# Kernel tuning notes

Hardware: AMD Instinct MI355X
Metric: run time of the kernel (lower is better)

## Reference

```python
import jax, jax.numpy as jnp
import numpy as np

P, B, N, M, D_LAT = 4, 32, 2048, 512, 128
BETA = 1e-3
BIG = 1e9  # sentinel for masked-out pairwise distances


def quat_to_rotmat(q):
    # q: (..., 4) quaternion (w, x, y, z), normalized then converted
    q = q / jnp.linalg.norm(q, axis=-1, keepdims=True)
    w, x, y, z = q[..., 0], q[..., 1], q[..., 2], q[..., 3]
    R = jnp.stack([
        1 - 2 * (y * y + z * z), 2 * (x * y - w * z), 2 * (x * z + w * y),
        2 * (x * y + w * z), 1 - 2 * (x * x + z * z), 2 * (y * z - w * x),
        2 * (x * z - w * y), 2 * (y * z + w * x), 1 - 2 * (x * x + y * y),
    ], axis=-1)
    return R.reshape(q.shape[:-1] + (3, 3))


def setup_inputs() -> dict:
    key = jax.random.key(0)
    ks = jax.random.split(key, 8)
    return {
        'ipt': jax.random.normal(ks[0], (B, N, 3), jnp.float32),
        'opt': jax.random.normal(ks[1], (P, B, M, 3), jnp.float32),
        'trans': jax.random.normal(ks[2], (P, B, 3), jnp.float32),
        'rots': jax.random.normal(ks[3], (P, B, 4), jnp.float32),
        'probs': jax.random.uniform(ks[4], (P, B, 1), jnp.float32),
        'idx': jax.random.randint(ks[5], (B, N), 0, P),
        'mu': jax.random.normal(ks[6], (B, D_LAT), jnp.float32),
        'logvar': jax.random.normal(ks[7], (B, D_LAT), jnp.float32),
    }


def _parts_distance(ipt, opt, trans, rots, probs, idx):
    # Masked, fully-batched equivalent of the original python double loop:
    # index_select by (idx==i) + _remove_zero_rows are expressed as boolean
    # masks; empty part/sample combinations are excluded via `valid`.
    chamfer_d = 0.0
    coverage = 0.0
    quality = 0.0
    num = 0.0
    nonzero_x = jnp.any(ipt != 0, axis=-1)  # (B, N)
    for i in range(P):  # fixed small part count, structurally distinct slices
        y = opt[i]                                   # (B, M, 3)
        mask_y = jnp.any(y != 0, axis=-1)            # (B, M) _remove_zero_rows
        mx = (idx == i) & nonzero_x                  # (B, N) part selection
        # transform_to_primitives_centric_system: x_local = R (x - t)
        R = quat_to_rotmat(rots[i])                  # (B, 3, 3)
        x = jnp.einsum('bij,bnj->bni', R, ipt - trans[i][:, None, :])
        # pairwise squared distances, (B, N, M)
        D = jnp.sum((x[:, :, None, :] - y[:, None, :, :]) ** 2, axis=-1)
        nx = jnp.sum(mx, axis=-1)                    # (B,)
        ny = jnp.sum(mask_y, axis=-1)                # (B,)
        # quality: mean over valid x of min distance to valid y
        qual = jnp.sum(jnp.where(mx, jnp.min(jnp.where(mask_y[:, None, :], D, BIG), axis=-1), 0.0), axis=-1) / jnp.maximum(nx, 1)
        # coverage: mean over valid y of min distance to valid x
        cov = jnp.sum(jnp.where(mask_y, jnp.min(jnp.where(mx[:, :, None], D, BIG), axis=-2), 0.0), axis=-1) / jnp.maximum(ny, 1)
        cd = qual + cov                              # symmetric chamfer
        valid = (nx > 0) & (ny > 0)                  # x.size(0)!=0 and y.size(0)!=0
        w = jnp.where(valid, probs[i][:, 0], 0.0)    # prob-weighted sum over batch
        n = jnp.sum(valid).astype(jnp.float32)
        has = (n > 0).astype(jnp.float32)
        inv_n = has / jnp.maximum(n, 1.0)
        chamfer_d = chamfer_d + jnp.sum(w * cd) * inv_n
        coverage = coverage + jnp.sum(w * cov) * inv_n
        quality = quality + jnp.sum(w * qual) * inv_n
        num = num + has
    inv_num = 1.0 / jnp.maximum(num, 1.0)
    return chamfer_d * inv_num, coverage * inv_num, quality * inv_num


def KL(mu, logvar):
    # standard VAE KL: sum over latent, mean over batch
    return -0.5 * jnp.sum(1.0 + logvar - mu ** 2 - jnp.exp(logvar)) / mu.shape[0]


def reference(ipt, opt, trans, rots, probs, idx, mu, logvar):
    cds, covs, quals = _parts_distance(ipt, opt, trans, rots, probs, idx)
    kld = KL(mu, logvar)
    return (cds + BETA * kld, cds, covs, quals, kld)
```

## Files before the change

### kernel.cpp

```cpp
#include <hip/hip_runtime.h>
#include <math.h>

#define PP 4
#define BB 32
#define NN 2048
#define MM 512
#define DLAT 128
#define BETA_C 1e-3f
#define BIGV 1e9f
#define SENT 1e8f
#define THREADS 256

__device__ float g_ws[4 * PP * BB];

template<int SLOTS>
__device__ __forceinline__ float quality_pass(
    const float* __restrict__ syx, const float* __restrict__ syy, const float* __restrict__ syz,
    const float* __restrict__ sxx, const float* __restrict__ sxy, const float* __restrict__ sxz,
    int nx, int base, int tid)
{
    float px[SLOTS], py[SLOTS], pz[SLOTS], mna[SLOTS], mnb[SLOTS];
    bool act[SLOTS];
#pragma unroll
    for (int s = 0; s < SLOTS; ++s) {
        int k = base + s * THREADS + tid;
        act[s] = (k < nx);
        px[s] = act[s] ? sxx[k] : SENT;
        py[s] = act[s] ? sxy[k] : SENT;
        pz[s] = act[s] ? sxz[k] : SENT;
        mna[s] = BIGV; mnb[s] = BIGV;
    }
    for (int m = 0; m < MM; m += 4) {
        float4 yx = *reinterpret_cast<const float4*>(syx + m);
        float4 yy = *reinterpret_cast<const float4*>(syy + m);
        float4 yz = *reinterpret_cast<const float4*>(syz + m);
#pragma unroll
        for (int s = 0; s < SLOTS; ++s) {
            float dx0 = px[s] - yx.x, dy0 = py[s] - yy.x, dz0 = pz[s] - yz.x;
            float dx1 = px[s] - yx.y, dy1 = py[s] - yy.y, dz1 = pz[s] - yz.y;
            float dx2 = px[s] - yx.z, dy2 = py[s] - yy.z, dz2 = pz[s] - yz.z;
            float dx3 = px[s] - yx.w, dy3 = py[s] - yy.w, dz3 = pz[s] - yz.w;
            float d0 = dx0 * dx0 + dy0 * dy0 + dz0 * dz0;
            float d1 = dx1 * dx1 + dy1 * dy1 + dz1 * dz1;
            float d2 = dx2 * dx2 + dy2 * dy2 + dz2 * dz2;
            float d3 = dx3 * dx3 + dy3 * dy3 + dz3 * dz3;
            mna[s] = fminf(mna[s], fminf(d0, d1));
            mnb[s] = fminf(mnb[s], fminf(d2, d3));
        }
    }
    float sum = 0.0f;
#pragma unroll
    for (int s = 0; s < SLOTS; ++s)
        if (act[s]) sum += fminf(mna[s], mnb[s]);
    return sum;
}

__device__ __forceinline__ float coverage_pass(
    const float* __restrict__ syx, const float* __restrict__ syy, const float* __restrict__ syz,
    const float* __restrict__ sxx, const float* __restrict__ sxy, const float* __restrict__ sxz,
    int nx4, int tid)
{
    float qx[2], qy[2], qz[2], mna[2], mnb[2];
#pragma unroll
    for (int s = 0; s < 2; ++s) {
        int m = s * THREADS + tid;
        qx[s] = syx[m]; qy[s] = syy[m]; qz[s] = syz[m];
        mna[s] = BIGV; mnb[s] = BIGV;
    }
    for (int k = 0; k < nx4; k += 4) {
        float4 xx = *reinterpret_cast<const float4*>(sxx + k);
        float4 xy = *reinterpret_cast<const float4*>(sxy + k);
        float4 xz = *reinterpret_cast<const float4*>(sxz + k);
#pragma unroll
        for (int s = 0; s < 2; ++s) {
            float dx0 = qx[s] - xx.x, dy0 = qy[s] - xy.x, dz0 = qz[s] - xz.x;
            float dx1 = qx[s] - xx.y, dy1 = qy[s] - xy.y, dz1 = qz[s] - xz.y;
            float dx2 = qx[s] - xx.z, dy2 = qy[s] - xy.z, dz2 = qz[s] - xz.z;
            float dx3 = qx[s] - xx.w, dy3 = qy[s] - xy.w, dz3 = qz[s] - xz.w;
            float d0 = dx0 * dx0 + dy0 * dy0 + dz0 * dz0;
            float d1 = dx1 * dx1 + dy1 * dy1 + dz1 * dz1;
            float d2 = dx2 * dx2 + dy2 * dy2 + dz2 * dz2;
            float d3 = dx3 * dx3 + dy3 * dy3 + dz3 * dz3;
            mna[s] = fminf(mna[s], fminf(d0, d1));
            mnb[s] = fminf(mnb[s], fminf(d2, d3));
        }
    }
    float sum = 0.0f;
#pragma unroll
    for (int s = 0; s < 2; ++s)
        if (qx[s] != SENT)
            sum += fminf(mna[s], mnb[s]);
    return sum;
}

__global__ __launch_bounds__(THREADS) void parts_kernel(
    const float* __restrict__ ipt,
    const float* __restrict__ opt,
    const float* __restrict__ trans,
    const float* __restrict__ rots,
    const int*   __restrict__ idx)
{
    const int b = blockIdx.x;
    const int i = blockIdx.y;
    const int phase = blockIdx.z;
    const int tid = threadIdx.x;

    __shared__ float Rm[12];
    __shared__ int s_nx, s_ny;
    __shared__ __align__(16) float syx[MM], syy[MM], syz[MM];
    __shared__ __align__(16) float sxx[NN], sxy[NN], sxz[NN];
    __shared__ float red[THREADS / 64];

    if (tid == 0) {
        s_nx = 0;
        s_ny = 0;
        const float* q = rots + (i * BB + b) * 4;
        float qw = q[0], qx = q[1], qy = q[2], qz = q[3];
        float inv = 1.0f / sqrtf(qw * qw + qx * qx + qy * qy + qz * qz);
        qw *= inv; qx *= inv; qy *= inv; qz *= inv;
        Rm[0] = 1.0f - 2.0f * (qy * qy + qz * qz);
        Rm[1] = 2.0f * (qx * qy - qw * qz);
        Rm[2] = 2.0f * (qx * qz + qw * qy);
        Rm[3] = 2.0f * (qx * qy + qw * qz);
        Rm[4] = 1.0f - 2.0f * (qx * qx + qz * qz);
        Rm[5] = 2.0f * (qy * qz - qw * qx);
        Rm[6] = 2.0f * (qx * qz - qw * qy);
        Rm[7] = 2.0f * (qy * qz + qw * qx);
        Rm[8] = 1.0f - 2.0f * (qx * qx + qy * qy);
        const float* t = trans + (i * BB + b) * 3;
        Rm[9] = t[0]; Rm[10] = t[1]; Rm[11] = t[2];
    }
    __syncthreads();

    int cnt = 0;
    for (int m = tid; m < MM; m += THREADS) {
        const float* y = opt + (((size_t)i * BB + b) * MM + m) * 3;
        float yx = y[0], yy = y[1], yz = y[2];
        bool v = (yx != 0.0f) | (yy != 0.0f) | (yz != 0.0f);
        if (v) cnt++;
        else { yx = SENT; yy = SENT; yz = SENT; }
        syx[m] = yx; syy[m] = yy; syz[m] = yz;
    }
    if (cnt) atomicAdd(&s_ny, cnt);

    const float R0 = Rm[0], R1 = Rm[1], R2 = Rm[2];
    const float R3 = Rm[3], R4 = Rm[4], R5 = Rm[5];
    const float R6 = Rm[6], R7 = Rm[7], R8 = Rm[8];
    const float t0 = Rm[9], t1 = Rm[10], t2 = Rm[11];
    for (int n = tid; n < NN; n += THREADS) {
        const float* p = ipt + ((size_t)b * NN + n) * 3;
        float px = p[0], py = p[1], pz = p[2];
        bool nz = (px != 0.0f) | (py != 0.0f) | (pz != 0.0f);
        if (nz && idx[b * NN + n] == i) {
            px -= t0; py -= t1; pz -= t2;
            int pos = atomicAdd(&s_nx, 1);
            sxx[pos] = R0 * px + R1 * py + R2 * pz;
            sxy[pos] = R3 * px + R4 * py + R5 * pz;
            sxz[pos] = R6 * px + R7 * py + R8 * pz;
        }
    }
    __syncthreads();
    const int nx = s_nx;
    const int ny = s_ny;
    const int nx4 = (nx + 3) & ~3;
    if (tid < nx4 - nx) {
        sxx[nx + tid] = SENT; sxy[nx + tid] = SENT; sxz[nx + tid] = SENT;
    }
    __syncthreads();

    float sum;
    if (phase == 0) {
        if (nx <= 2 * THREADS) {
            sum = quality_pass<2>(syx, syy, syz, sxx, sxy, sxz, nx, 0, tid);
        } else {
            sum = quality_pass<3>(syx, syy, syz, sxx, sxy, sxz, nx, 0, tid);
            for (int k0 = 3 * THREADS; k0 < nx; k0 += THREADS)
                sum += quality_pass<1>(syx, syy, syz, sxx, sxy, sxz, nx, k0, tid);
        }
    } else {
        sum = coverage_pass(syx, syy, syz, sxx, sxy, sxz, nx4, tid);
    }

    for (int off = 32; off > 0; off >>= 1) sum += __shfl_down(sum, off);
    if ((tid & 63) == 0) red[tid >> 6] = sum;
    __syncthreads();
    if (tid == 0) {
        float tot = 0.0f;
        for (int w = 0; w < THREADS / 64; ++w) tot += red[w];
        int pb = i * BB + b;
        if (phase == 0) {
            g_ws[pb] = tot;
            g_ws[2 * PP * BB + pb] = (float)nx;
        } else {
            g_ws[PP * BB + pb] = tot;
            g_ws[3 * PP * BB + pb] = (float)ny;
        }
    }
}

__global__ __launch_bounds__(256) void finalize_kernel(
    const float* __restrict__ probs,
    const float* __restrict__ mu,
    const float* __restrict__ logvar,
    float* __restrict__ out)
{
    const int tid = threadIdx.x;
    __shared__ float red[4];
    __shared__ float s_wq[PP * BB], s_wc[PP * BB], s_val[PP * BB];

    float kls = 0.0f;
    for (int t = tid; t < BB * DLAT; t += 256) {
        float m_ = mu[t], lv = logvar[t];
        kls += 1.0f + lv - m_ * m_ - expf(lv);
    }
    for (int off = 32; off > 0; off >>= 1) kls += __shfl_down(kls, off);
    if ((tid & 63) == 0) red[tid >> 6] = kls;

    if (tid < PP * BB) {
        float qs = g_ws[tid];
        float cs = g_ws[PP * BB + tid];
        float nxf = g_ws[2 * PP * BB + tid];
        float nyf = g_ws[3 * PP * BB + tid];
        bool valid = (nxf > 0.0f) && (nyf > 0.0f);
        float w = valid ? probs[tid] : 0.0f;
        s_wq[tid] = w * (qs / fmaxf(nxf, 1.0f));
        s_wc[tid] = w * (cs / fmaxf(nyf, 1.0f));
        s_val[tid] = valid ? 1.0f : 0.0f;
    }
    __syncthreads();

    if (tid == 0) {
        float kld = -0.5f * (red[0] + red[1] + red[2] + red[3]) / (float)BB;
        float ch = 0.0f, cov = 0.0f, qu = 0.0f, num = 0.0f;
        for (int i = 0; i < PP; ++i) {
            float sq = 0.0f, sc = 0.0f, n = 0.0f;
            for (int bb = 0; bb < BB; ++bb) {
                sq += s_wq[i * BB + bb];
                sc += s_wc[i * BB + bb];
                n += s_val[i * BB + bb];
            }
            float has = (n > 0.0f) ? 1.0f : 0.0f;
            float invn = has / fmaxf(n, 1.0f);
            qu += sq * invn;
            cov += sc * invn;
            ch += (sq + sc) * invn;
            num += has;
        }
        float invnum = 1.0f / fmaxf(num, 1.0f);
        float cds = ch * invnum;
        out[0] = cds + BETA_C * kld;
        out[1] = cds;
        out[2] = cov * invnum;
        out[3] = qu * invnum;
        out[4] = kld;
    }
}

extern "C" void kernel_launch(void* const* d_in, const int* in_sizes, int n_in,
                              void* d_out, int out_size, void* d_ws, size_t ws_size,
                              hipStream_t stream) {
    const float* ipt    = (const float*)d_in[0];
    const float* opt    = (const float*)d_in[1];
    const float* trans  = (const float*)d_in[2];
    const float* rots   = (const float*)d_in[3];
    const float* probs  = (const float*)d_in[4];
    const int*   idx    = (const int*)d_in[5];
    const float* mu     = (const float*)d_in[6];
    const float* logvar = (const float*)d_in[7];
    float* out = (float*)d_out;
    (void)d_ws; (void)ws_size; (void)in_sizes; (void)n_in; (void)out_size;

    dim3 grid(BB, PP, 2);
    parts_kernel<<<grid, THREADS, 0, stream>>>(ipt, opt, trans, rots, idx);
    finalize_kernel<<<1, 256, 0, stream>>>(probs, mu, logvar, out);
}
```

Before: 110.2 us.

## Split quality and coverage passes into chunks for more blocks

Each (part, batch) pair's quality pass now covers half of the input points and each coverage pass covers half of the output points. This doubles the grid to 512 blocks to fill more compute units, and the partial sums and counts are combined in the finalize kernel. In exchange every block redundantly reloads and filters the inputs, and coverage blocks still scan all gathered points.

```diff
diff --git a/kernel.cpp b/kernel.cpp
--- a/kernel.cpp
+++ b/kernel.cpp
@@ -3,6 +3,7 @@
 
 #define PP 4
 #define BB 32
+#define PB (PP * BB)
 #define NN 2048
 #define MM 512
 #define DLAT 128
@@ -10,8 +11,11 @@
 #define BIGV 1e9f
 #define SENT 1e8f
 #define THREADS 256
-
-__device__ float g_ws[4 * PP * BB];
+#define NCHUNK 2
+#define QCH (NN / NCHUNK)
+#define CCH (MM / NCHUNK)
+
+__device__ float g_ws[8 * PB];
 
 template<int SLOTS>
 __device__ __forceinline__ float quality_pass(
@@ -55,44 +59,6 @@
     return sum;
 }
 
-__device__ __forceinline__ float coverage_pass(
-    const float* __restrict__ syx, const float* __restrict__ syy, const float* __restrict__ syz,
-    const float* __restrict__ sxx, const float* __restrict__ sxy, const float* __restrict__ sxz,
-    int nx4, int tid)
-{
-    float qx[2], qy[2], qz[2], mna[2], mnb[2];
-#pragma unroll
-    for (int s = 0; s < 2; ++s) {
-        int m = s * THREADS + tid;
-        qx[s] = syx[m]; qy[s] = syy[m]; qz[s] = syz[m];
-        mna[s] = BIGV; mnb[s] = BIGV;
-    }
-    for (int k = 0; k < nx4; k += 4) {
-        float4 xx = *reinterpret_cast<const float4*>(sxx + k);
-        float4 xy = *reinterpret_cast<const float4*>(sxy + k);
-        float4 xz = *reinterpret_cast<const float4*>(sxz + k);
-#pragma unroll
-        for (int s = 0; s < 2; ++s) {
-            float dx0 = qx[s] - xx.x, dy0 = qy[s] - xy.x, dz0 = qz[s] - xz.x;
-            float dx1 = qx[s] - xx.y, dy1 = qy[s] - xy.y, dz1 = qz[s] - xz.y;
-            float dx2 = qx[s] - xx.z, dy2 = qy[s] - xy.z, dz2 = qz[s] - xz.z;
-            float dx3 = qx[s] - xx.w, dy3 = qy[s] - xy.w, dz3 = qz[s] - xz.w;
-            float d0 = dx0 * dx0 + dy0 * dy0 + dz0 * dz0;
-            float d1 = dx1 * dx1 + dy1 * dy1 + dz1 * dz1;
-            float d2 = dx2 * dx2 + dy2 * dy2 + dz2 * dz2;
-            float d3 = dx3 * dx3 + dy3 * dy3 + dz3 * dz3;
-            mna[s] = fminf(mna[s], fminf(d0, d1));
-            mnb[s] = fminf(mnb[s], fminf(d2, d3));
-        }
-    }
-    float sum = 0.0f;
-#pragma unroll
-    for (int s = 0; s < 2; ++s)
-        if (qx[s] != SENT)
-            sum += fminf(mna[s], mnb[s]);
-    return sum;
-}
-
 __global__ __launch_bounds__(THREADS) void parts_kernel(
     const float* __restrict__ ipt,
     const float* __restrict__ opt,
@@ -102,7 +68,7 @@
 {
     const int b = blockIdx.x;
     const int i = blockIdx.y;
-    const int phase = blockIdx.z;
+    const int z = blockIdx.z;
     const int tid = threadIdx.x;
 
     __shared__ float Rm[12];
@@ -132,68 +98,112 @@
     }
     __syncthreads();
 
-    int cnt = 0;
-    for (int m = tid; m < MM; m += THREADS) {
-        const float* y = opt + (((size_t)i * BB + b) * MM + m) * 3;
-        float yx = y[0], yy = y[1], yz = y[2];
-        bool v = (yx != 0.0f) | (yy != 0.0f) | (yz != 0.0f);
-        if (v) cnt++;
-        else { yx = SENT; yy = SENT; yz = SENT; }
-        syx[m] = yx; syy[m] = yy; syz[m] = yz;
-    }
-    if (cnt) atomicAdd(&s_ny, cnt);
-
     const float R0 = Rm[0], R1 = Rm[1], R2 = Rm[2];
     const float R3 = Rm[3], R4 = Rm[4], R5 = Rm[5];
     const float R6 = Rm[6], R7 = Rm[7], R8 = Rm[8];
     const float t0 = Rm[9], t1 = Rm[10], t2 = Rm[11];
-    for (int n = tid; n < NN; n += THREADS) {
-        const float* p = ipt + ((size_t)b * NN + n) * 3;
-        float px = p[0], py = p[1], pz = p[2];
-        bool nz = (px != 0.0f) | (py != 0.0f) | (pz != 0.0f);
-        if (nz && idx[b * NN + n] == i) {
-            px -= t0; py -= t1; pz -= t2;
-            int pos = atomicAdd(&s_nx, 1);
-            sxx[pos] = R0 * px + R1 * py + R2 * pz;
-            sxy[pos] = R3 * px + R4 * py + R5 * pz;
-            sxz[pos] = R6 * px + R7 * py + R8 * pz;
-        }
-    }
-    __syncthreads();
-    const int nx = s_nx;
-    const int ny = s_ny;
-    const int nx4 = (nx + 3) & ~3;
-    if (tid < nx4 - nx) {
-        sxx[nx + tid] = SENT; sxy[nx + tid] = SENT; sxz[nx + tid] = SENT;
-    }
-    __syncthreads();
-
-    float sum;
-    if (phase == 0) {
-        if (nx <= 2 * THREADS) {
-            sum = quality_pass<2>(syx, syy, syz, sxx, sxy, sxz, nx, 0, tid);
+    const size_t optbase = ((size_t)i * BB + b) * MM;
+    const int pb = i * BB + b;
+
+    if (z < NCHUNK) {
+        for (int m = tid; m < MM; m += THREADS) {
+            const float* y = opt + (optbase + m) * 3;
+            float yx = y[0], yy = y[1], yz = y[2];
+            bool v = (yx != 0.0f) | (yy != 0.0f) | (yz != 0.0f);
+            if (!v) { yx = SENT; yy = SENT; yz = SENT; }
+            syx[m] = yx; syy[m] = yy; syz[m] = yz;
+        }
+        const int n0 = z * QCH;
+        for (int n = n0 + tid; n < n0 + QCH; n += THREADS) {
+            const float* p = ipt + ((size_t)b * NN + n) * 3;
+            float px = p[0], py = p[1], pz = p[2];
+            bool nz = (px != 0.0f) | (py != 0.0f) | (pz != 0.0f);
+            if (nz && idx[b * NN + n] == i) {
+                px -= t0; py -= t1; pz -= t2;
+                int pos = atomicAdd(&s_nx, 1);
+                sxx[pos] = R0 * px + R1 * py + R2 * pz;
+                sxy[pos] = R3 * px + R4 * py + R5 * pz;
+                sxz[pos] = R6 * px + R7 * py + R8 * pz;
+            }
+        }
+        __syncthreads();
+        const int nxc = s_nx;
+
+        float sum;
+        if (nxc <= THREADS) {
+            sum = quality_pass<1>(syx, syy, syz, sxx, sxy, sxz, nxc, 0, tid);
+        } else if (nxc <= 2 * THREADS) {
+            sum = quality_pass<2>(syx, syy, syz, sxx, sxy, sxz, nxc, 0, tid);
         } else {
-            sum = quality_pass<3>(syx, syy, syz, sxx, sxy, sxz, nx, 0, tid);
-            for (int k0 = 3 * THREADS; k0 < nx; k0 += THREADS)
-                sum += quality_pass<1>(syx, syy, syz, sxx, sxy, sxz, nx, k0, tid);
+            sum = quality_pass<2>(syx, syy, syz, sxx, sxy, sxz, nxc, 0, tid);
+            for (int k0 = 2 * THREADS; k0 < nxc; k0 += THREADS)
+                sum += quality_pass<1>(syx, syy, syz, sxx, sxy, sxz, nxc, k0, tid);
+        }
+
+        for (int off = 32; off > 0; off >>= 1) sum += __shfl_down(sum, off);
+        if ((tid & 63) == 0) red[tid >> 6] = sum;
+        __syncthreads();
+        if (tid == 0) {
+            float tot = red[0] + red[1] + red[2] + red[3];
+            g_ws[(0 + z) * PB + pb] = tot;
+            g_ws[(4 + z) * PB + pb] = (float)nxc;
         }
     } else {
-        sum = coverage_pass(syx, syy, syz, sxx, sxy, sxz, nx4, tid);
-    }
-
-    for (int off = 32; off > 0; off >>= 1) sum += __shfl_down(sum, off);
-    if ((tid & 63) == 0) red[tid >> 6] = sum;
-    __syncthreads();
-    if (tid == 0) {
-        float tot = 0.0f;
-        for (int w = 0; w < THREADS / 64; ++w) tot += red[w];
-        int pb = i * BB + b;
-        if (phase == 0) {
-            g_ws[pb] = tot;
-            g_ws[2 * PP * BB + pb] = (float)nx;
-        } else {
-            g_ws[PP * BB + pb] = tot;
-            g_ws[3 * PP * BB + pb] = (float)ny;
+        const int c = z - NCHUNK;
+        const int m = c * CCH + tid;
+        const float* y = opt + (optbase + m) * 3;
+        float qx = y[0], qy = y[1], qz = y[2];
+        bool v = (qx != 0.0f) | (qy != 0.0f) | (qz != 0.0f);
+        if (!v) { qx = SENT; qy = SENT; qz = SENT; }
+        unsigned long long bal = __ballot(v);
+        if ((tid & 63) == 0) atomicAdd(&s_ny, __popcll(bal));
+
+        for (int n = tid; n < NN; n += THREADS) {
+            const float* p = ipt + ((size_t)b * NN + n) * 3;
+            float px = p[0], py = p[1], pz = p[2];
+            bool nz = (px != 0.0f) | (py != 0.0f) | (pz != 0.0f);
+            if (nz && idx[b * NN + n] == i) {
+                px -= t0; py -= t1; pz -= t2;
+                int pos = atomicAdd(&s_nx, 1);
+                sxx[pos] = R0 * px + R1 * py + R2 * pz;
+                sxy[pos] = R3 * px + R4 * py + R5 * pz;
+                sxz[pos] = R6 * px + R7 * py + R8 * pz;
+            }
+        }
+        __syncthreads();
+        const int nx = s_nx;
+        const int ny = s_ny;
+        const int nx4 = (nx + 3) & ~3;
+        if (tid < nx4 - nx) {
+            sxx[nx + tid] = SENT; sxy[nx + tid] = SENT; sxz[nx + tid] = SENT;
+        }
+        __syncthreads();
+
+        float mna = BIGV, mnb = BIGV;
+        for (int k = 0; k < nx4; k += 4) {
+            float4 xx = *reinterpret_cast<const float4*>(sxx + k);
+            float4 xy = *reinterpret_cast<const float4*>(sxy + k);
+            float4 xz = *reinterpret_cast<const float4*>(sxz + k);
+            float dx0 = qx - xx.x, dy0 = qy - xy.x, dz0 = qz - xz.x;
+            float dx1 = qx - xx.y, dy1 = qy - xy.y, dz1 = qz - xz.y;
+            float dx2 = qx - xx.z, dy2 = qy - xy.z, dz2 = qz - xz.z;
+            float dx3 = qx - xx.w, dy3 = qy - xy.w, dz3 = qz - xz.w;
+            float d0 = dx0 * dx0 + dy0 * dy0 + dz0 * dz0;
+            float d1 = dx1 * dx1 + dy1 * dy1 + dz1 * dz1;
+            float d2 = dx2 * dx2 + dy2 * dy2 + dz2 * dz2;
+            float d3 = dx3 * dx3 + dy3 * dy3 + dz3 * dz3;
+            mna = fminf(mna, fminf(d0, d1));
+            mnb = fminf(mnb, fminf(d2, d3));
+        }
+        float sum = v ? fminf(mna, mnb) : 0.0f;
+
+        for (int off = 32; off > 0; off >>= 1) sum += __shfl_down(sum, off);
+        if ((tid & 63) == 0) red[tid >> 6] = sum;
+        __syncthreads();
+        if (tid == 0) {
+            float tot = red[0] + red[1] + red[2] + red[3];
+            g_ws[(2 + c) * PB + pb] = tot;
+            g_ws[(6 + c) * PB + pb] = (float)ny;
         }
     }
 }
@@ -206,7 +216,7 @@
 {
     const int tid = threadIdx.x;
     __shared__ float red[4];
-    __shared__ float s_wq[PP * BB], s_wc[PP * BB], s_val[PP * BB];
+    __shared__ float s_wq[PB], s_wc[PB], s_val[PB];
 
     float kls = 0.0f;
     for (int t = tid; t < BB * DLAT; t += 256) {
@@ -216,11 +226,11 @@
     for (int off = 32; off > 0; off >>= 1) kls += __shfl_down(kls, off);
     if ((tid & 63) == 0) red[tid >> 6] = kls;
 
-    if (tid < PP * BB) {
-        float qs = g_ws[tid];
-        float cs = g_ws[PP * BB + tid];
-        float nxf = g_ws[2 * PP * BB + tid];
-        float nyf = g_ws[3 * PP * BB + tid];
+    if (tid < PB) {
+        float qs  = g_ws[0 * PB + tid] + g_ws[1 * PB + tid];
+        float cs  = g_ws[2 * PB + tid] + g_ws[3 * PB + tid];
+        float nxf = g_ws[4 * PB + tid] + g_ws[5 * PB + tid];
+        float nyf = g_ws[6 * PB + tid] + g_ws[7 * PB + tid];
         bool valid = (nxf > 0.0f) && (nyf > 0.0f);
         float w = valid ? probs[tid] : 0.0f;
         s_wq[tid] = w * (qs / fmaxf(nxf, 1.0f));
@@ -270,7 +280,7 @@
     float* out = (float*)d_out;
     (void)d_ws; (void)ws_size; (void)in_sizes; (void)n_in; (void)out_size;
 
-    dim3 grid(BB, PP, 2);
+    dim3 grid(BB, PP, 2 * NCHUNK);
     parts_kernel<<<grid, THREADS, 0, stream>>>(ipt, opt, trans, rots, idx);
     finalize_kernel<<<1, 256, 0, stream>>>(probs, mu, logvar, out);
 }
```

Measured after the change: 98.86 us. 1.12x faster.
